# Optimization experiments

Measured on AMD Instinct MI355X. Metric: run time of the kernel, lower is better.

Reference implementation:

```python
import jax, jax.numpy as jnp
import numpy as np

DOF = 7
B = 8192
DT = 0.1
ACTION_RANGE = 50.0
MAX_VEL = 20.0


def _skew(w):
    x, y, z = w[..., 0], w[..., 1], w[..., 2]
    O = jnp.zeros_like(x)
    return jnp.stack([jnp.stack([O, -z, y], -1),
                      jnp.stack([z, O, -x], -1),
                      jnp.stack([-y, x, O], -1)], -2)


def _exp_se3(xi):
    # xi: (..., 6) twist [w; v] (already scaled by joint angle) -> (..., 4, 4)
    w, v = xi[..., :3], xi[..., 3:]
    th = jnp.sqrt(jnp.sum(w * w, -1))
    small = th < 1e-4
    ths = jnp.where(small, 1.0, th)  # safe denominator
    th2 = th * th
    a = jnp.where(small, 1.0 - th2 / 6.0, jnp.sin(th) / ths)
    b = jnp.where(small, 0.5 - th2 / 24.0, (1.0 - jnp.cos(th)) / (ths * ths))
    c = jnp.where(small, 1.0 / 6.0 - th2 / 120.0, (th - jnp.sin(th)) / (ths * ths * ths))
    K = _skew(w)
    K2 = K @ K
    I3 = jnp.eye(3, dtype=xi.dtype)
    R = I3 + a[..., None, None] * K + b[..., None, None] * K2
    Vm = I3 + b[..., None, None] * K + c[..., None, None] * K2
    p = jnp.einsum('...ij,...j->...i', Vm, v)
    top = jnp.concatenate([R, p[..., None]], -1)
    bot = jnp.broadcast_to(jnp.array([0.0, 0.0, 0.0, 1.0], xi.dtype), top.shape[:-2] + (1, 4))
    return jnp.concatenate([top, bot], -2)


def _inv_T(T):
    R = T[..., :3, :3]
    p = T[..., :3, 3]
    Rt = jnp.swapaxes(R, -1, -2)
    pn = -jnp.einsum('...ij,...j->...i', Rt, p)
    top = jnp.concatenate([Rt, pn[..., None]], -1)
    bot = jnp.broadcast_to(jnp.array([0.0, 0.0, 0.0, 1.0], T.dtype), top.shape[:-2] + (1, 4))
    return jnp.concatenate([top, bot], -2)


def _adjoint(T):
    # SE(3) adjoint for [w; v] twists: [[R, 0], [ [p]x R, R ]]
    R = T[..., :3, :3]
    p = T[..., :3, 3]
    pR = _skew(p) @ R
    Z = jnp.zeros_like(R)
    return jnp.concatenate([jnp.concatenate([R, Z], -1),
                            jnp.concatenate([pR, R], -1)], -2)


def _ad(V):
    # se(3) little adjoint: [[ [w]x, 0 ], [ [v]x, [w]x ]]
    Kw = _skew(V[..., :3])
    Kv = _skew(V[..., 3:])
    Z = jnp.zeros_like(Kw)
    return jnp.concatenate([jnp.concatenate([Kw, Z], -1),
                            jnp.concatenate([Kv, Kw], -1)], -2)


def _inverse_dynamics(q, dq, ddq, g, Ftip, M, G, A):
    # Recursive Newton-Euler (Modern Robotics, link-frame screws A).
    Bq, n = q.shape
    V = jnp.zeros((Bq, 6), q.dtype)
    Vd = jnp.broadcast_to(jnp.concatenate([jnp.zeros(3, q.dtype), -g]), (Bq, 6))
    AdTs, Vs, Vds = [], [], []
    for i in range(n):
        T = _exp_se3(-A[i] * q[:, i, None]) @ _inv_T(M[i])  # T_{i,i-1}, (B,4,4)
        AdT = _adjoint(T)
        V = jnp.einsum('bij,bj->bi', AdT, V) + A[i] * dq[:, i, None]
        Vd = (jnp.einsum('bij,bj->bi', AdT, Vd)
              + jnp.einsum('bij,j->bi', _ad(V), A[i]) * dq[:, i, None]
              + A[i] * ddq[:, i, None])
        AdTs.append(AdT)
        Vs.append(V)
        Vds.append(Vd)
    F = jnp.broadcast_to(Ftip.astype(q.dtype), (Bq, 6))
    AdT_end = _adjoint(_inv_T(M[n]))  # T_{n+1,n}, (6,6)
    taus = [None] * n
    for i in range(n - 1, -1, -1):
        if i == n - 1:
            F = jnp.einsum('ji,bj->bi', AdT_end, F)
        else:
            F = jnp.einsum('bji,bj->bi', AdTs[i + 1], F)
        F = (F + jnp.einsum('ij,bj->bi', G[i], Vds[i])
             - jnp.einsum('bji,jk,bk->bi', _ad(Vs[i]), G[i], Vs[i]))
        taus[i] = jnp.einsum('bi,i->b', F, A[i])
    return jnp.stack(taus, -1)  # (B, n)


def _forward_dynamics(q, dq, tau, g, Ftip, M, G, A):
    n = q.shape[1]
    zer = jnp.zeros_like(q)
    # bias forces: Coriolis + gravity + end-effector wrench
    h = _inverse_dynamics(q, dq, zer, g, Ftip, M, G, A)
    g0 = jnp.zeros(3, q.dtype)
    f0 = jnp.zeros(6, q.dtype)
    # mass matrix columns via unit accelerations (vmapped over columns)
    cols = jax.vmap(lambda e: _inverse_dynamics(
        q, zer, jnp.broadcast_to(e, q.shape), g0, f0, M, G, A))(jnp.eye(n, dtype=q.dtype))
    Mmat = jnp.transpose(cols, (1, 2, 0))  # (B, n, n)
    return jnp.linalg.solve(Mmat, (tau - h)[..., None])[..., 0]


def _fk_in_space(q, M, A):
    Bq, n = q.shape
    T = jnp.broadcast_to(jnp.eye(4, dtype=q.dtype), (Bq, 4, 4))
    outs = []
    for i in range(n):
        T = (T @ M[i]) @ _exp_se3(A[i] * q[:, i, None])
        outs.append(T)
    outs.append(T @ M[n])
    return jnp.stack(outs, 1)  # (B, n+1, 4, 4)


def setup_inputs():
    key = jax.random.key(0)
    ks = jax.random.split(key, 4)
    state = jax.random.normal(ks[0], (B, 2 * DOF), jnp.float32)
    torque = jax.random.normal(ks[1], (B, DOF), jnp.float32)
    M = jnp.tile(jnp.eye(4, dtype=jnp.float32)[None], (DOF + 1, 1, 1))
    A = jax.random.uniform(ks[2], (DOF, 6), jnp.float32)
    L = jax.random.normal(ks[3], (DOF, 6, 6), jnp.float32)
    gravity = jnp.array([0.0, -9.8, 0.0], jnp.float32)
    ftip = jnp.zeros(6, jnp.float32)
    return {"state": state, "torque": torque, "M": M, "A": A, "L": L,
            "gravity": gravity, "ftip": ftip}


def reference(state, torque, M, A, L, gravity, ftip):
    n = DOF
    G = L @ jnp.swapaxes(L, -1, -2)  # spatial inertias, PSD
    s0 = jnp.concatenate([state, torque * ACTION_RANGE], -1)  # (B, 3n)

    def derivs(s):
        q = s[..., :n]
        dq = s[..., n:2 * n]
        qf = s[..., 2 * n:]
        qacc = _forward_dynamics(q, dq, qf, gravity, ftip, M, G, A)
        return jnp.concatenate([dq, qacc, jnp.zeros_like(qf)], -1)

    k1 = derivs(s0)
    k2 = derivs(s0 + 0.5 * DT * k1)
    k3 = derivs(s0 + 0.5 * DT * k2)
    k4 = derivs(s0 + DT * k3)
    s1 = s0 + (DT / 6.0) * (k1 + 2.0 * k2 + 2.0 * k3 + k4)
    q = jnp.mod(s1[..., :n] + jnp.pi, 2.0 * jnp.pi) - jnp.pi
    dq = jnp.clip(s1[..., n:2 * n], -MAX_VEL, MAX_VEL)
    ee = _fk_in_space(q, M, A)
    return jnp.concatenate([q, dq], -1), ee[:, -1, :2, 3]
```

## Files before the change

kernel.cpp:

```cpp
#include <hip/hip_runtime.h>
#include <hip/hip_bf16.h>

#define DTC 0.1f
#define ACTION_RANGE 50.0f
#define MAX_VEL 20.0f
#define PI_F 3.14159265358979323846f
#define TWO_PI_F 6.28318530717958647692f
#define INV_TWO_PI_F 0.15915494309189533577f

__device__ __forceinline__ float bf2f(__hip_bfloat16 x){ return __bfloat162float(x); }

__device__ __forceinline__ float ldv(const void* p, int i, bool isb){
  return isb ? __bfloat162float(((const __hip_bfloat16*)p)[i]) : ((const float*)p)[i];
}
__device__ __forceinline__ void stv(void* p, int i, float v, bool isb){
  if (isb) ((__hip_bfloat16*)p)[i] = __float2bfloat16(v);
  else     ((float*)p)[i] = v;
}

__device__ __forceinline__ void exp_se3_Rp(const float* Aj, float s, float* R, float* P){
  float wx=Aj[0]*s, wy=Aj[1]*s, wz=Aj[2]*s;
  float vx=Aj[3]*s, vy=Aj[4]*s, vz=Aj[5]*s;
  float th2 = wx*wx+wy*wy+wz*wz;
  float th = sqrtf(th2);
  float a,b,c;
  if (th < 0.25f){
    float th4 = th2*th2;
    a = 1.f - th2*(1.f/6.f) + th4*(1.f/120.f);
    b = 0.5f - th2*(1.f/24.f) + th4*(1.f/720.f);
    c = (1.f/6.f) - th2*(1.f/120.f) + th4*(1.f/5040.f);
  } else {
    float sn = sinf(th), cs = cosf(th);
    float inv = 1.f/th, inv2 = inv*inv;
    a = sn*inv;
    b = (1.f-cs)*inv2;
    c = (th-sn)*inv2*inv;
  }
  R[0]=1.f+b*(wx*wx-th2); R[1]=b*wx*wy-a*wz;      R[2]=b*wx*wz+a*wy;
  R[3]=b*wx*wy+a*wz;      R[4]=1.f+b*(wy*wy-th2); R[5]=b*wy*wz-a*wx;
  R[6]=b*wx*wz-a*wy;      R[7]=b*wy*wz+a*wx;      R[8]=1.f+b*(wz*wz-th2);
  float V0=1.f+c*(wx*wx-th2), V1=c*wx*wy-b*wz,      V2=c*wx*wz+b*wy;
  float V3=c*wx*wy+b*wz,      V4=1.f+c*(wy*wy-th2), V5=c*wy*wz-b*wx;
  float V6=c*wx*wz-b*wy,      V7=c*wy*wz+b*wx,      V8=1.f+c*(wz*wz-th2);
  P[0]=V0*vx+V1*vy+V2*vz;
  P[1]=V3*vx+V4*vy+V5*vz;
  P[2]=V6*vx+V7*vy+V8*vz;
}

__device__ __forceinline__ void mul33(const float* X, const float* Y, float* Z){
  #pragma unroll
  for (int r=0;r<3;r++){
    float x0=X[r*3+0], x1=X[r*3+1], x2=X[r*3+2];
    Z[r*3+0]=x0*Y[0]+x1*Y[3]+x2*Y[6];
    Z[r*3+1]=x0*Y[1]+x1*Y[4]+x2*Y[7];
    Z[r*3+2]=x0*Y[2]+x1*Y[5]+x2*Y[8];
  }
}

__device__ __forceinline__ void ad_apply(const float* R, const float* p, const float* Vin, float* Vout){
  float i0=Vin[0],i1=Vin[1],i2=Vin[2],i3=Vin[3],i4=Vin[4],i5=Vin[5];
  float w0 = R[0]*i0+R[1]*i1+R[2]*i2;
  float w1 = R[3]*i0+R[4]*i1+R[5]*i2;
  float w2 = R[6]*i0+R[7]*i1+R[8]*i2;
  float r0 = R[0]*i3+R[1]*i4+R[2]*i5;
  float r1 = R[3]*i3+R[4]*i4+R[5]*i5;
  float r2 = R[6]*i3+R[7]*i4+R[8]*i5;
  float p0=p[0],p1=p[1],p2=p[2];
  Vout[0]=w0; Vout[1]=w1; Vout[2]=w2;
  Vout[3]=p1*w2-p2*w1+r0;
  Vout[4]=p2*w0-p0*w2+r1;
  Vout[5]=p0*w1-p1*w0+r2;
}

__device__ __forceinline__ void adT_apply(const float* R, const float* p, const float* Fin, float* Fout){
  float m0=Fin[0],m1=Fin[1],m2=Fin[2],f0=Fin[3],f1=Fin[4],f2=Fin[5];
  float p0=p[0],p1=p[1],p2=p[2];
  float cx = m0 - (p1*f2 - p2*f1);
  float cy = m1 - (p2*f0 - p0*f2);
  float cz = m2 - (p0*f1 - p1*f0);
  float o0 = R[0]*cx + R[3]*cy + R[6]*cz;
  float o1 = R[1]*cx + R[4]*cy + R[7]*cz;
  float o2 = R[2]*cx + R[5]*cy + R[8]*cz;
  float o3 = R[0]*f0 + R[3]*f1 + R[6]*f2;
  float o4 = R[1]*f0 + R[4]*f1 + R[7]*f2;
  float o5 = R[2]*f0 + R[5]*f1 + R[8]*f2;
  Fout[0]=o0;Fout[1]=o1;Fout[2]=o2;Fout[3]=o3;Fout[4]=o4;Fout[5]=o5;
}

__device__ __forceinline__ void gmatvec(const float* G, const float* v, float* out){
  float v0=v[0],v1=v[1],v2=v[2],v3=v[3],v4=v[4],v5=v[5];
  #pragma unroll
  for (int r=0;r<6;r++)
    out[r] = G[r*6+0]*v0+G[r*6+1]*v1+G[r*6+2]*v2+G[r*6+3]*v3+G[r*6+4]*v4+G[r*6+5]*v5;
}

#define W_STRIDE 85

__global__ __launch_bounds__(64) void arm_rk4_kernel(
    const void* __restrict__ g_state,
    const void* __restrict__ g_torque,
    const void* __restrict__ g_M,
    const void* __restrict__ g_A,
    const void* __restrict__ g_L,
    const void* __restrict__ g_grav,
    const void* __restrict__ g_ftip,
    void* __restrict__ g_out,
    int B)
{
  __shared__ float sA[42];
  __shared__ float sG[252];
  __shared__ float sMinvR[72];
  __shared__ float sMinvp[24];
  __shared__ float sMR[72];
  __shared__ float sMp[24];
  __shared__ float sgrav[3];
  __shared__ float sftip[6];
  __shared__ float sW[8*W_STRIDE];

  const bool isb = fabsf(bf2f(((const __hip_bfloat16*)g_grav)[1]) + 9.8f) < 0.5f;

  const int t = threadIdx.x;
  for (int x=t; x<42; x+=64) sA[x] = ldv(g_A, x, isb);
  for (int x=t; x<252; x+=64){
    int i = x/36; int rc = x - i*36; int rr = rc/6; int cc = rc - rr*6;
    float s = 0.f;
    #pragma unroll
    for (int k=0;k<6;k++) s += ldv(g_L, i*36+rr*6+k, isb) * ldv(g_L, i*36+cc*6+k, isb);
    sG[x] = s;
  }
  if (t < 8){
    float R[9], p[3];
    #pragma unroll
    for (int rr=0;rr<3;rr++){
      #pragma unroll
      for (int cc=0;cc<3;cc++) R[rr*3+cc] = ldv(g_M, t*16 + rr*4 + cc, isb);
      p[rr] = ldv(g_M, t*16 + rr*4 + 3, isb);
    }
    #pragma unroll
    for (int rr=0;rr<3;rr++){
      #pragma unroll
      for (int cc=0;cc<3;cc++){ sMR[t*9+rr*3+cc] = R[rr*3+cc]; sMinvR[t*9+rr*3+cc] = R[cc*3+rr]; }
      sMp[t*3+rr] = p[rr];
      sMinvp[t*3+rr] = -(R[0*3+rr]*p[0] + R[1*3+rr]*p[1] + R[2*3+rr]*p[2]);
    }
  }
  if (t == 0){ for (int k=0;k<3;k++) sgrav[k] = ldv(g_grav, k, isb); }
  if (t == 1){ for (int k=0;k<6;k++) sftip[k] = ldv(g_ftip, k, isb); }
  __syncthreads();

  const int e = t >> 3;
  const int r = t & 7;
  int b = blockIdx.x * 8 + e;
  if (b >= B) b = B - 1;
  const bool is7 = (r == 7);
  float* W = &sW[e*W_STRIDE];

  float q0[7], dq0[7], qf[7];
  #pragma unroll
  for (int i=0;i<7;i++){
    q0[i]  = ldv(g_state, b*14+i, isb);
    dq0[i] = ldv(g_state, b*14+7+i, isb);
    qf[i]  = ldv(g_torque, b*7+i, isb) * ACTION_RANGE;
  }
  float kq[7], kdd[7], accq[7], accdq[7];
  #pragma unroll
  for (int i=0;i<7;i++){ kq[i]=0.f; kdd[i]=0.f; accq[i]=0.f; accdq[i]=0.f; }

  float Fend[6];
  {
    float tf[6]; adT_apply(&sMinvR[63], &sMinvp[21], sftip, tf);
    #pragma unroll
    for (int k=0;k<6;k++) Fend[k] = is7 ? tf[k] : 0.f;
  }

  #pragma unroll 1
  for (int st=0; st<4; ++st){
    const float cin = (st==0) ? 0.f : ((st==3) ? DTC : 0.5f*DTC);
    const float wgt = (st==0||st==3) ? (DTC/6.f) : (DTC/3.f);
    float qs[7], dqs[7];
    #pragma unroll
    for (int i=0;i<7;i++){ qs[i]=q0[i]+cin*kq[i]; dqs[i]=dq0[i]+cin*kdd[i]; }

    float qsr = 0.f;
    #pragma unroll
    for (int c=0;c<7;c++) qsr = (r==c) ? qs[c] : qsr;

    if (r < 7){
      float Re[9], Pe[3], Rt[9];
      exp_se3_Rp(&sA[r*6], -qsr, Re, Pe);
      mul33(Re, &sMinvR[r*9], Rt);
      #pragma unroll
      for (int k=0;k<9;k++) W[r*12+k] = Rt[k];
      #pragma unroll
      for (int rr=0;rr<3;rr++)
        W[r*12+9+rr] = Re[rr*3+0]*sMinvp[r*3+0] + Re[rr*3+1]*sMinvp[r*3+1]
                     + Re[rr*3+2]*sMinvp[r*3+2] + Pe[rr];
    }
    __syncthreads();

    float Va[7][6], Vda[7][6];
    float V[6] = {0,0,0,0,0,0};
    float Vd[6];
    Vd[0]=0.f; Vd[1]=0.f; Vd[2]=0.f;
    Vd[3] = is7 ? -sgrav[0] : 0.f;
    Vd[4] = is7 ? -sgrav[1] : 0.f;
    Vd[5] = is7 ? -sgrav[2] : 0.f;
    #pragma unroll
    for (int i=0;i<7;i++){
      const float* R = &W[i*12];
      const float* p = R+9;
      float dqi  = is7 ? dqs[i] : 0.f;
      float ddqi = is7 ? 0.f : ((r==i) ? 1.f : 0.f);
      ad_apply(R,p,V,V);
      #pragma unroll
      for (int k=0;k<6;k++) V[k] += sA[i*6+k]*dqi;
      ad_apply(R,p,Vd,Vd);
      {
        float w0=V[0],w1=V[1],w2=V[2],v0=V[3],v1=V[4],v2=V[5];
        float a0=sA[i*6+0],a1=sA[i*6+1],a2=sA[i*6+2],a3=sA[i*6+3],a4=sA[i*6+4],a5=sA[i*6+5];
        Vd[0] += (w1*a2-w2*a1)*dqi + a0*ddqi;
        Vd[1] += (w2*a0-w0*a2)*dqi + a1*ddqi;
        Vd[2] += (w0*a1-w1*a0)*dqi + a2*ddqi;
        Vd[3] += ((v1*a2-v2*a1)+(w1*a5-w2*a4))*dqi + a3*ddqi;
        Vd[4] += ((v2*a0-v0*a2)+(w2*a3-w0*a5))*dqi + a4*ddqi;
        Vd[5] += ((v0*a1-v1*a0)+(w0*a4-w1*a3))*dqi + a5*ddqi;
      }
      #pragma unroll
      for (int k=0;k<6;k++){ Va[i][k]=V[k]; Vda[i][k]=Vd[k]; }
    }

    float m[7];
    {
      float F[6];
      #pragma unroll
      for (int k=0;k<6;k++) F[k] = Fend[k];
      #pragma unroll
      for (int i=6;i>=0;i--){
        if (i<6) adT_apply(&W[(i+1)*12], &W[(i+1)*12+9], F, F);
        float gv[6], gvd[6];
        gmatvec(&sG[i*36], Va[i], gv);
        gmatvec(&sG[i*36], Vda[i], gvd);
        float w0=Va[i][0],w1=Va[i][1],w2=Va[i][2],v0=Va[i][3],v1=Va[i][4],v2=Va[i][5];
        F[0] += gvd[0] + (w1*gv[2]-w2*gv[1]) + (v1*gv[5]-v2*gv[4]);
        F[1] += gvd[1] + (w2*gv[0]-w0*gv[2]) + (v2*gv[3]-v0*gv[5]);
        F[2] += gvd[2] + (w0*gv[1]-w1*gv[0]) + (v0*gv[4]-v1*gv[3]);
        F[3] += gvd[3] + (w1*gv[5]-w2*gv[4]);
        F[4] += gvd[4] + (w2*gv[3]-w0*gv[5]);
        F[5] += gvd[5] + (w0*gv[4]-w1*gv[3]);
        m[i] = F[0]*sA[i*6+0]+F[1]*sA[i*6+1]+F[2]*sA[i*6+2]
             + F[3]*sA[i*6+3]+F[4]*sA[i*6+4]+F[5]*sA[i*6+5];
      }
    }

    float rhs = 0.f;
    #pragma unroll
    for (int c=0;c<7;c++){
      float hc = __shfl(m[c], 7, 8);
      rhs = (r==c) ? (qf[c]-hc) : rhs;
    }
    #pragma unroll
    for (int k=0;k<7;k++){
      float pvk   = __shfl(m[k], k, 8);
      float pvrhs = __shfl(rhs,  k, 8);
      float pinv  = 1.f/pvk;
      float f = (r>k) ? m[k]*pinv : 0.f;
      #pragma unroll
      for (int c=k+1;c<7;c++){
        float pvc = __shfl(m[c], k, 8);
        m[c] -= f*pvc;
      }
      rhs -= f*pvrhs;
    }
    float x[7];
    #pragma unroll
    for (int i=6;i>=0;i--){
      float di = __shfl(m[i], i, 8);
      float si = __shfl(rhs, i, 8);
      float xi = si/di;
      x[i] = xi;
      rhs -= ((r<i) ? m[i] : 0.f) * xi;
    }

    #pragma unroll
    for (int i=0;i<7;i++){
      kq[i]  = dqs[i];
      kdd[i] = x[i];
      accq[i]  += wgt*dqs[i];
      accdq[i] += wgt*x[i];
    }
    __syncthreads();
  }

  float q1[7], dq1[7];
  #pragma unroll
  for (int i=0;i<7;i++){
    float xx = q0[i] + accq[i] + PI_F;
    float mm = xx - floorf(xx * INV_TWO_PI_F) * TWO_PI_F;
    q1[i] = mm - PI_F;
    float dv = dq0[i] + accdq[i];
    dq1[i] = fminf(fmaxf(dv, -MAX_VEL), MAX_VEL);
  }

  float Rt[9] = {1.f,0.f,0.f, 0.f,1.f,0.f, 0.f,0.f,1.f};
  float Pt[3] = {0.f,0.f,0.f};
  #pragma unroll
  for (int i=0;i<7;i++){
    float tmp[9];
    float px = Rt[0]*sMp[i*3+0]+Rt[1]*sMp[i*3+1]+Rt[2]*sMp[i*3+2] + Pt[0];
    float py = Rt[3]*sMp[i*3+0]+Rt[4]*sMp[i*3+1]+Rt[5]*sMp[i*3+2] + Pt[1];
    float pz = Rt[6]*sMp[i*3+0]+Rt[7]*sMp[i*3+1]+Rt[8]*sMp[i*3+2] + Pt[2];
    mul33(Rt, &sMR[i*9], tmp);
    #pragma unroll
    for (int k=0;k<9;k++) Rt[k]=tmp[k];
    Pt[0]=px; Pt[1]=py; Pt[2]=pz;
    float Re[9], Pe[3];
    exp_se3_Rp(&sA[i*6], q1[i], Re, Pe);
    px = Rt[0]*Pe[0]+Rt[1]*Pe[1]+Rt[2]*Pe[2] + Pt[0];
    py = Rt[3]*Pe[0]+Rt[4]*Pe[1]+Rt[5]*Pe[2] + Pt[1];
    pz = Rt[6]*Pe[0]+Rt[7]*Pe[1]+Rt[8]*Pe[2] + Pt[2];
    mul33(Rt, Re, tmp);
    #pragma unroll
    for (int k=0;k<9;k++) Rt[k]=tmp[k];
    Pt[0]=px; Pt[1]=py; Pt[2]=pz;
  }
  float ex = Rt[0]*sMp[21]+Rt[1]*sMp[22]+Rt[2]*sMp[23] + Pt[0];
  float ey = Rt[3]*sMp[21]+Rt[4]*sMp[22]+Rt[5]*sMp[23] + Pt[1];

  float q1r=0.f, dq1r=0.f;
  #pragma unroll
  for (int c=0;c<7;c++){
    q1r  = (r==c) ? q1[c]  : q1r;
    dq1r = (r==c) ? dq1[c] : dq1r;
  }
  if (r < 7){
    stv(g_out, b*14+r,   q1r,  isb);
    stv(g_out, b*14+7+r, dq1r, isb);
  } else {
    stv(g_out, B*14 + b*2 + 0, ex, isb);
    stv(g_out, B*14 + b*2 + 1, ey, isb);
  }
}

extern "C" void kernel_launch(void* const* d_in, const int* in_sizes, int n_in,
                              void* d_out, int out_size, void* d_ws, size_t ws_size,
                              hipStream_t stream) {
  const int B = in_sizes[0] / 14;
  const int blocks = (B + 7) / 8;
  arm_rk4_kernel<<<blocks, 64, 0, stream>>>(d_in[0], d_in[1], d_in[2], d_in[3],
                                            d_in[4], d_in[5], d_in[6], d_out, B);
}
```

Baseline: 99.59 us.

## Use fast intrinsics in exp_se3 and solve mass matrix redundantly per lane

The exp_se3 coefficient computation drops the divergent branch. It now always evaluates the fast hardware sin, cos, sqrt and reciprocal intrinsics and picks the Taylor or closed form with selects. The 7x7 Gaussian elimination no longer runs distributed across 8 lanes with many shuffles per step. Instead every lane gathers the whole matrix with 49 shuffles and does elimination and back substitution redundantly in registers. This trades the serial shuffle dependency chains for more registers and duplicated arithmetic, and the fast intrinsics may lose some accuracy.

```diff
diff --git a/kernel.cpp b/kernel.cpp
--- a/kernel.cpp
+++ b/kernel.cpp
@@ -22,20 +22,16 @@
   float wx=Aj[0]*s, wy=Aj[1]*s, wz=Aj[2]*s;
   float vx=Aj[3]*s, vy=Aj[4]*s, vz=Aj[5]*s;
   float th2 = wx*wx+wy*wy+wz*wz;
-  float th = sqrtf(th2);
-  float a,b,c;
-  if (th < 0.25f){
-    float th4 = th2*th2;
-    a = 1.f - th2*(1.f/6.f) + th4*(1.f/120.f);
-    b = 0.5f - th2*(1.f/24.f) + th4*(1.f/720.f);
-    c = (1.f/6.f) - th2*(1.f/120.f) + th4*(1.f/5040.f);
-  } else {
-    float sn = sinf(th), cs = cosf(th);
-    float inv = 1.f/th, inv2 = inv*inv;
-    a = sn*inv;
-    b = (1.f-cs)*inv2;
-    c = (th-sn)*inv2*inv;
-  }
+  float th  = __builtin_amdgcn_sqrtf(th2);
+  float sn  = __sinf(th);
+  float cs  = __cosf(th);
+  float rth = __builtin_amdgcn_rcpf(fmaxf(th, 0.05f));
+  float rth2 = rth*rth;
+  float th4 = th2*th2;
+  bool small = th2 < 0.01f;
+  float a = small ? (1.f - th2*(1.f/6.f)  + th4*(1.f/120.f))  : sn*rth;
+  float b = small ? (0.5f - th2*(1.f/24.f) + th4*(1.f/720.f)) : (1.f-cs)*rth2;
+  float c = small ? ((1.f/6.f) - th2*(1.f/120.f) + th4*(1.f/5040.f)) : (th-sn)*rth*rth2;
   R[0]=1.f+b*(wx*wx-th2); R[1]=b*wx*wy-a*wz;      R[2]=b*wx*wz+a*wy;
   R[3]=b*wx*wy+a*wz;      R[4]=1.f+b*(wy*wy-th2); R[5]=b*wy*wz-a*wx;
   R[6]=b*wx*wz-a*wy;      R[7]=b*wy*wz+a*wx;      R[8]=1.f+b*(wz*wz-th2);
@@ -252,33 +248,33 @@
       }
     }
 
-    float rhs = 0.f;
+    float Mf[7][7], rhs[7];
     #pragma unroll
     for (int c=0;c<7;c++){
       float hc = __shfl(m[c], 7, 8);
-      rhs = (r==c) ? (qf[c]-hc) : rhs;
+      rhs[c] = qf[c] - hc;
+      #pragma unroll
+      for (int src=0;src<7;src++)
+        Mf[src][c] = __shfl(m[c], src, 8);
     }
     #pragma unroll
     for (int k=0;k<7;k++){
-      float pvk   = __shfl(m[k], k, 8);
-      float pvrhs = __shfl(rhs,  k, 8);
-      float pinv  = 1.f/pvk;
-      float f = (r>k) ? m[k]*pinv : 0.f;
-      #pragma unroll
-      for (int c=k+1;c<7;c++){
-        float pvc = __shfl(m[c], k, 8);
-        m[c] -= f*pvc;
+      float pinv = 1.f / Mf[k][k];
+      #pragma unroll
+      for (int rr=k+1;rr<7;rr++){
+        float f = Mf[rr][k] * pinv;
+        #pragma unroll
+        for (int c=k+1;c<7;c++) Mf[rr][c] -= f * Mf[k][c];
+        rhs[rr] -= f * rhs[k];
       }
-      rhs -= f*pvrhs;
     }
     float x[7];
     #pragma unroll
     for (int i=6;i>=0;i--){
-      float di = __shfl(m[i], i, 8);
-      float si = __shfl(rhs, i, 8);
-      float xi = si/di;
-      x[i] = xi;
-      rhs -= ((r<i) ? m[i] : 0.f) * xi;
+      float s = rhs[i];
+      #pragma unroll
+      for (int c=i+1;c<7;c++) s -= Mf[i][c] * x[c];
+      x[i] = s / Mf[i][i];
     }
 
     #pragma unroll
```

After: 109.5 us. 1.1x slower.
